# Performance work log

Hardware: AMD Instinct MI355X
Metric: run time of the kernel (lower is better)

Reference implementation:

```python
import jax, jax.numpy as jnp
import numpy as np

H = 128          # hidden_dim
L = 3            # num_layers
N = 100_000      # nodes
E = 1_600_000    # edges (avg degree 16)


def setup_inputs() -> dict:
    key = jax.random.key(0)
    ks = jax.random.split(key, 12)
    x = jax.random.normal(ks[0], (N, 5), dtype=jnp.float32)
    edge_index = jax.random.randint(ks[1], (2, E), 0, N, dtype=jnp.int64)
    edge_attr = jax.random.normal(ks[2], (E, 4), dtype=jnp.float32)

    def w(k, shape):
        fan_in = shape[-2]
        return (jax.random.normal(k, shape, dtype=jnp.float32) / np.sqrt(fan_in)).astype(jnp.float32)

    return {
        "x": x, "edge_index": edge_index, "edge_attr": edge_attr,
        # input_mlp: Linear(3,H) + SiLU
        "in_w": w(ks[3], (3, H)), "in_b": jnp.zeros((H,), jnp.float32),
        # per-layer edge_mlp: Linear(10,H) SiLU Linear(H,H), stacked over L layers
        "ew1": w(ks[4], (L, 10, H)), "eb1": jnp.zeros((L, H), jnp.float32),
        "ew2": w(ks[5], (L, H, H)), "eb2": jnp.zeros((L, H), jnp.float32),
        # per-layer node_mlp: Linear(2H,H) SiLU Linear(H,H)
        "nw1": w(ks[6], (L, 2 * H, H)), "nb1": jnp.zeros((L, H), jnp.float32),
        "nw2": w(ks[7], (L, H, H)), "nb2": jnp.zeros((L, H), jnp.float32),
        # output_mlp: Linear(H,H) SiLU Linear(H,1)
        "ow1": w(ks[8], (H, H)), "ob1": jnp.zeros((H,), jnp.float32),
        "ow2": w(ks[9], (H, 1)), "ob2": jnp.zeros((1,), jnp.float32),
    }


def reference(x, edge_index, edge_attr,
              in_w, in_b,
              ew1, eb1, ew2, eb2,
              nw1, nb1, nw2, nb2,
              ow1, ob1, ow2, ob2):
    n = x.shape[0]
    src, dst = edge_index[0], edge_index[1]  # PyG: j=src=edge_index[0], i=dst=edge_index[1]

    node_type = x[:, :2]
    spins = x[:, 2:5]
    # F.normalize(spins, dim=1) with eps=1e-12
    spins = spins / jnp.maximum(jnp.linalg.norm(spins, axis=-1, keepdims=True), 1e-12)
    spin_norm = jnp.linalg.norm(spins, axis=-1, keepdims=True)

    h = jax.nn.silu(jnp.concatenate([node_type, spin_norm], axis=-1) @ in_w + in_b)  # [N,H]

    # per-edge scalar invariants: layer-independent, compute once. [E,10]
    m_i, m_j = spins[dst], spins[src]
    nt_i, nt_j = node_type[dst], node_type[src]
    unit_vec = edge_attr[:, :3]
    distance = edge_attr[:, 3:4]
    scalars = jnp.concatenate([
        jnp.linalg.norm(m_i, axis=-1, keepdims=True),
        jnp.linalg.norm(m_j, axis=-1, keepdims=True),
        jnp.sum(m_i * m_j, axis=-1, keepdims=True),
        jnp.sum(m_i * unit_vec, axis=-1, keepdims=True),
        jnp.sum(m_j * unit_vec, axis=-1, keepdims=True),
        distance, nt_i, nt_j], axis=-1)

    def layer(h, p):
        w1, b1, w2, b2, mw1, mb1, mw2, mb2 = p
        msg = jax.nn.silu(scalars @ w1 + b1) @ w2 + b2            # [E,H] edge MLP
        aggr = jax.ops.segment_sum(msg, dst, num_segments=n)      # scatter-add to dst
        upd = jax.nn.silu(jnp.concatenate([h, aggr], -1) @ mw1 + mb1) @ mw2 + mb2
        return h + upd, None                                      # residual

    h, _ = jax.lax.scan(layer, h, (ew1, eb1, ew2, eb2, nw1, nb1, nw2, nb2))

    weights = jax.nn.silu(h @ ow1 + ob1) @ ow2 + ob2               # [N,1]
    contrib = weights[src] * spins[src]                            # [E,3]
    b_field = jax.ops.segment_sum(contrib, dst, num_segments=n)    # [N,3]
    return b_field
```

## Files before the change

kernel.cpp:

```cpp
#include <hip/hip_runtime.h>
#include <hip/hip_bf16.h>
#include <math.h>

typedef __attribute__((ext_vector_type(8))) short bf16x8;
typedef __attribute__((ext_vector_type(4))) float f32x4;
typedef __attribute__((ext_vector_type(4))) unsigned u32x4;

#define C_NLOG2E -1.4426950408889634f
#define C_NLN2   -0.6931471805599453f

__device__ __forceinline__ float silu_f(float x){
  return x * __builtin_amdgcn_rcpf(1.f + __expf(-x));
}

__device__ __forceinline__ void silu_acc(float h, float& s){
  float r = __builtin_amdgcn_rcpf(1.f + __builtin_amdgcn_exp2f(h));
  s = fmaf(h, r, s);
}

__device__ __forceinline__ short f2bs(float x){
  unsigned u = __builtin_bit_cast(unsigned, x);
  unsigned r = (u + 0x7fffu + ((u >> 16) & 1u)) >> 16;
  return (short)r;
}
__device__ __forceinline__ float bs2f(ushort u){
  unsigned v = ((unsigned)u) << 16;
  return __builtin_bit_cast(float, v);
}

__global__ void k_detect(const int* __restrict__ ei, int E, int* __restrict__ flag){
  __shared__ int nz;
  if (threadIdx.x==0) nz = 0;
  __syncthreads();
  int lim = E < 4096 ? E : 4096;
  int c = 0;
  for (int e = threadIdx.x; e < lim; e += blockDim.x)
    if (ei[2*e+1] != 0) c++;
  if (c) atomicAdd(&nz, c);
  __syncthreads();
  if (threadIdx.x==0) *flag = (nz==0) ? 1 : 0;
}

__global__ __launch_bounds__(256) void k_deg(const int* __restrict__ ei, int E,
                                             const int* __restrict__ flag, int* __restrict__ deg){
  int e = blockIdx.x*blockDim.x + threadIdx.x;
  if (e >= E) return;
  int d = (*flag) ? ei[2*(E+e)] : ei[E+e];
  atomicAdd(&deg[d], 1);
}

__global__ __launch_bounds__(256) void k_scan1(const int* __restrict__ deg, int* __restrict__ offs,
                                               int* __restrict__ bsum,
                                               const float* __restrict__ x, float4* __restrict__ nrec,
                                               int n){
  __shared__ int sh[256];
  int i = blockIdx.x*256 + threadIdx.x;
  int v = (i < n) ? deg[i] : 0;
  sh[threadIdx.x] = v;
  if (i < n){
    float nt0 = x[i*5+0], nt1 = x[i*5+1];
    float sx = x[i*5+2], sy = x[i*5+3], sz = x[i*5+4];
    float nrm = sqrtf(sx*sx + sy*sy + sz*sz);
    float d = fmaxf(nrm, 1e-12f);
    float mx = sx/d, my = sy/d, mz = sz/d;
    float rn = sqrtf(mx*mx + my*my + mz*mz);
    nrec[(size_t)i*2]   = make_float4(mx, my, mz, rn);
    nrec[(size_t)i*2+1] = make_float4(nt0, nt1, 0.f, 0.f);
  }
  __syncthreads();
  for (int off=1; off<256; off<<=1){
    int t = (threadIdx.x >= off) ? sh[threadIdx.x-off] : 0;
    __syncthreads();
    sh[threadIdx.x] += t;
    __syncthreads();
  }
  if (i < n) offs[i] = sh[threadIdx.x] - v;
  if (threadIdx.x == 255) bsum[blockIdx.x] = sh[255];
}

__global__ __launch_bounds__(512) void k_scan2(int* __restrict__ bsum, int nb){
  __shared__ int sh[512];
  int v = (threadIdx.x < nb) ? bsum[threadIdx.x] : 0;
  sh[threadIdx.x] = v;
  __syncthreads();
  for (int off=1; off<512; off<<=1){
    int t = (threadIdx.x >= off) ? sh[threadIdx.x-off] : 0;
    __syncthreads();
    sh[threadIdx.x] += t;
    __syncthreads();
  }
  if (threadIdx.x < nb) bsum[threadIdx.x] = sh[threadIdx.x] - v;
}

__global__ __launch_bounds__(256) void k_scan3(int* __restrict__ offs, const int* __restrict__ bsum,
                                               int* __restrict__ cursor,
                                               const int* __restrict__ deg,
                                               int* __restrict__ cnt, int4* __restrict__ c4,
                                               int4* __restrict__ c8, int n){
  int i = blockIdx.x*256 + threadIdx.x;
  if (i >= n) return;
  int o = offs[i] + bsum[i>>8];
  offs[i] = o;
  cursor[i] = o;
  int d = deg[i];
  int r = d & 15;
  if (r == 0 || r >= 9) return;
  int base = o + (d & ~15);
  if (r <= 4){
    int s = atomicAdd(&cnt[0], 1);
    c4[s] = make_int4(i, base, r, 0);
  } else {
    int s = atomicAdd(&cnt[1], 2);
    c8[s]   = make_int4(i, base, 4, 0);
    c8[s+1] = make_int4(i, base+4, r-4, 0);
  }
}

__global__ __launch_bounds__(256) void k_scatter(const int* __restrict__ ei, int E,
                                                 const int* __restrict__ flag,
                                                 const float* __restrict__ eattr,
                                                 const float4* __restrict__ nrec,
                                                 int* __restrict__ cursor,
                                                 int* __restrict__ srcS, ushort* __restrict__ scE){
  int e = blockIdx.x*blockDim.x + threadIdx.x;
  if (e >= E) return;
  int i64 = *flag;
  int s = i64 ? ei[2*e]       : ei[e];
  int d = i64 ? ei[2*(E+e)]   : ei[E+e];
  float4 ea = *(const float4*)(eattr + (size_t)e*4);
  float4 mi  = nrec[(size_t)d*2];
  float4 nti = nrec[(size_t)d*2+1];
  float4 mj  = nrec[(size_t)s*2];
  float4 ntj = nrec[(size_t)s*2+1];
  __align__(16) ushort row[16];
  row[0] = (ushort)f2bs(mi.w);
  row[1] = (ushort)f2bs(mj.w);
  row[2] = (ushort)f2bs(mi.x*mj.x + mi.y*mj.y + mi.z*mj.z);
  row[3] = (ushort)f2bs(mi.x*ea.x + mi.y*ea.y + mi.z*ea.z);
  row[4] = (ushort)f2bs(mj.x*ea.x + mj.y*ea.y + mj.z*ea.z);
  row[5] = (ushort)f2bs(ea.w);
  row[6] = (ushort)f2bs(nti.x);
  row[7] = (ushort)f2bs(nti.y);
  row[8] = (ushort)f2bs(ntj.x);
  row[9] = (ushort)f2bs(ntj.y);
  row[10]= 0x3F80;
  row[11]=0; row[12]=0; row[13]=0; row[14]=0; row[15]=0;
  int pos = atomicAdd(&cursor[d], 1);
  srcS[pos] = s;
  u32x4* dstp = (u32x4*)(scE + (size_t)pos*16);
  dstp[0] = *(u32x4*)row;
  dstp[1] = *(u32x4*)(row + 8);
}

__global__ __launch_bounds__(64) void k_pack(const float* __restrict__ ew2, const float* __restrict__ nw1,
                                             const float* __restrict__ nw2, const float* __restrict__ ow1,
                                             const float* __restrict__ ew1, const float* __restrict__ eb1,
                                             short* __restrict__ p_ew2, short* __restrict__ p_nw1,
                                             short* __restrict__ p_nw2, short* __restrict__ p_ow1,
                                             short* __restrict__ p_ew1){
  int b = blockIdx.x;
  int L = threadIdx.x;
  if (b >= 416){
    int tile = b - 416;
    int l = tile >> 3, t = tile & 7;
    int col = t*16 + (L & 15);
    int kb  = (L >> 4) << 3;
    __align__(16) short tmp[8];
    #pragma unroll
    for (int e=0;e<8;e++){
      int k = kb + e;
      float v = 0.f;
      if (k < 10)       v = ew1[(size_t)l*1280 + (size_t)k*128 + col];
      else if (k == 10) v = eb1[(size_t)l*128 + col];
      tmp[e] = f2bs(v * C_NLOG2E);
    }
    *(bf16x8*)(p_ew1 + (size_t)l*4096 + t*512 + L*8) = *(bf16x8*)tmp;
    return;
  }
  const float* src; short* dst; int tile;
  float sc = 1.f;
  if (b < 96){        int l = b>>5;              tile = b & 31; src = ew2 + (size_t)l*16384; dst = p_ew2 + (size_t)l*16384; sc = C_NLN2; }
  else if (b < 288){  int l = (b-96)>>6;         tile = (b-96) & 63; src = nw1 + (size_t)l*32768; dst = p_nw1 + (size_t)l*32768; }
  else if (b < 384){  int l = (b-288)>>5;        tile = (b-288) & 31; src = nw2 + (size_t)l*16384; dst = p_nw2 + (size_t)l*16384; }
  else {                                          tile = b - 384; src = ow1; dst = p_ow1; }
  int c = tile >> 3, t = tile & 7;
  int kb  = c*32 + ((L>>4)<<3);
  int col = t*16 + (L&15);
  __align__(16) short tmp[8];
  #pragma unroll
  for (int e=0;e<8;e++) tmp[e] = f2bs(src[(size_t)(kb+e)*128 + col] * sc);
  *(bf16x8*)(dst + ((size_t)tile*64 + L)*8) = *(bf16x8*)tmp;
}

__global__ __launch_bounds__(256) void k_edge3(
    const ushort* __restrict__ scE,
    const int* __restrict__ offs, const int* __restrict__ deg,
    const short* __restrict__ p_ew1,
    ushort* __restrict__ A, int n, size_t lstride){
  int wv = threadIdx.x >> 6, lane = threadIdx.x & 63;
  int i = blockIdx.x*4 + wv;
  if (i >= n) return;
  int quad = lane >> 4, lr = lane & 15;
  int p0 = __builtin_amdgcn_readfirstlane(offs[i]);
  int dg = __builtin_amdgcn_readfirstlane(deg[i]);
  int r  = dg & 15;
  int gfull = dg & ~15;
  const f32x4 zf = {0.f,0.f,0.f,0.f};
  const u32x4 z4 = {0u,0u,0u,0u};
  #pragma unroll 1
  for (int l=0; l<3; ++l){
    const short* pB = p_ew1 + (size_t)l*4096 + (size_t)lane*8;
    bf16x8 bfr[8];
    #pragma unroll
    for (int t=0;t<8;t++) bfr[t] = *(const bf16x8*)(pB + t*512);
    float s8[8];
    #pragma unroll
    for (int t=0;t<8;t++) s8[t] = 0.f;
    auto body = [&](u32x4 d4){
      bf16x8 af = __builtin_bit_cast(bf16x8, d4);
      #pragma unroll
      for (int t=0;t<8;t++){
        f32x4 acc = __builtin_amdgcn_mfma_f32_16x16x32_bf16(af, bfr[t], zf, 0, 0, 0);
        silu_acc(acc[0], s8[t]);
        silu_acc(acc[1], s8[t]);
        silu_acc(acc[2], s8[t]);
        silu_acc(acc[3], s8[t]);
      }
    };
    for (int g=0; g<gfull; g+=16){
      u32x4 d4 = z4;
      if (quad < 2)
        d4 = *(const u32x4*)(scE + ((size_t)(p0+g+lr))*16 + quad*8);
      body(d4);
    }
    if (r >= 9){
      int e = gfull + lr;
      u32x4 d4 = z4;
      if (quad < 2 && e < dg)
        d4 = *(const u32x4*)(scE + ((size_t)(p0+e))*16 + quad*8);
      body(d4);
    }
    #pragma unroll
    for (int t=0;t<8;t++){
      s8[t] += __shfl_xor(s8[t], 16, 64);
      s8[t] += __shfl_xor(s8[t], 32, 64);
    }
    if (quad == 0){
      #pragma unroll
      for (int t=0;t<8;t++)
        A[lstride*l + (size_t)i*128 + t*16 + lr] = (ushort)f2bs(s8[t]);
    }
  }
}

__global__ __launch_bounds__(256) void k_edge_rem(
    const ushort* __restrict__ scE,
    const int* __restrict__ cnt,
    const int4* __restrict__ c4, const int4* __restrict__ c8,
    const short* __restrict__ p_ew1,
    ushort* __restrict__ A, size_t lstride, int T4){
  int wave = threadIdx.x >> 6, lane = threadIdx.x & 63;
  int tw = blockIdx.x*4 + wave;
  const int4* slots;
  int mode;
  if (tw < T4){
    if (tw*4 >= cnt[0]) return;
    slots = c4 + (size_t)tw*4; mode = 0;
  } else {
    int t2 = tw - T4;
    if (t2*4 >= cnt[1]) return;
    slots = c8 + (size_t)t2*4; mode = 1;
  }
  int lr = lane & 15, quad = lane >> 4;
  int4 sl = slots[lr >> 2];
  int4 so = slots[quad];
  u32x4 d4 = {0u,0u,0u,0u};
  if (quad < 2 && (lr & 3) < sl.z)
    d4 = *(const u32x4*)(scE + (size_t)(sl.y + (lr & 3))*16 + quad*8);
  bf16x8 af = __builtin_bit_cast(bf16x8, d4);
  const f32x4 zf = {0.f,0.f,0.f,0.f};
  bool writer = (so.x >= 0) && (mode == 0 || (quad & 1) == 0);
  #pragma unroll 1
  for (int l=0; l<3; ++l){
    const short* pB = p_ew1 + (size_t)l*4096 + (size_t)lane*8;
    float s8[8];
    #pragma unroll
    for (int t=0;t<8;t++){
      bf16x8 bf = *(const bf16x8*)(pB + t*512);
      f32x4 acc = __builtin_amdgcn_mfma_f32_16x16x32_bf16(af, bf, zf, 0, 0, 0);
      float s = 0.f;
      silu_acc(acc[0], s);
      silu_acc(acc[1], s);
      silu_acc(acc[2], s);
      silu_acc(acc[3], s);
      s8[t] = s;
    }
    if (mode == 1){
      #pragma unroll
      for (int t=0;t<8;t++) s8[t] += __shfl_xor(s8[t], 16, 64);
    }
    if (writer){
      ushort* Ar = A + lstride*l + (size_t)so.x*128;
      #pragma unroll
      for (int t=0;t<8;t++){
        int col = t*16 + lr;
        Ar[col] = (ushort)f2bs(bs2f(Ar[col]) + s8[t]);
      }
    }
  }
}

__device__ __forceinline__ void wave_gemm2(const short* __restrict__ s0, const short* __restrict__ s1,
                                           const short* __restrict__ pw, int lane,
                                           f32x4 acc0[8], f32x4 acc1[8]){
  int lro = (lane & 15)*136 + ((lane >> 4) << 3);
  #pragma unroll
  for (int c=0;c<4;c++){
    bf16x8 a0 = *(const bf16x8*)(s0 + lro + c*32);
    bf16x8 a1 = *(const bf16x8*)(s1 + lro + c*32);
    const short* pB = pw + (size_t)c*4096 + (size_t)lane*8;
    #pragma unroll
    for (int t=0;t<8;t++){
      bf16x8 bf = *(const bf16x8*)(pB + t*512);
      acc0[t] = __builtin_amdgcn_mfma_f32_16x16x32_bf16(a0, bf, acc0[t], 0, 0, 0);
      acc1[t] = __builtin_amdgcn_mfma_f32_16x16x32_bf16(a1, bf, acc1[t], 0, 0, 0);
    }
  }
}

__global__ __launch_bounds__(64,2) void k_layers(
    const ushort* __restrict__ A, size_t lstride,
    const short* __restrict__ p_ew2, const float* __restrict__ eb2,
    const short* __restrict__ p_nw1, const float* __restrict__ nb1,
    const short* __restrict__ p_nw2, const float* __restrict__ nb2,
    const int* __restrict__ deg,
    const short* __restrict__ p_ow1, const float* __restrict__ ob1,
    const float* __restrict__ ow2, const float* __restrict__ ob2,
    const float* __restrict__ inw, const float* __restrict__ inb,
    const float4* __restrict__ nrec, float4* __restrict__ wspin, int n){
  __shared__ __align__(16) short sH[2][2176];
  __shared__ __align__(16) short sG[2][2176];
  int lane = threadIdx.x;
  int lr = lane & 15, quad = lane >> 4, qrow = quad << 2;
  int b0 = blockIdx.x*32;
  int b1 = b0 + 16;

  const f32x4 zf = {0.f,0.f,0.f,0.f};
  const bf16x8 zb = {0,0,0,0,0,0,0,0};
  f32x4 h0a[8], h1a[8];
  f32x4 acc0[8], acc1[8];
  bool rv0 = (b0 + lr) < n, rv1 = (b1 + lr) < n;
  float dd0[4], dd1[4];

  {
    float nt0a[4], nt1a[4], rna[4], nt0b[4], nt1b[4], rnb[4];
    #pragma unroll
    for (int r=0;r<4;r++){
      int ra = b0 + qrow + r, rb = b1 + qrow + r;
      if (ra < n){
        float4 a = nrec[(size_t)ra*2]; float4 b = nrec[(size_t)ra*2+1];
        nt0a[r]=b.x; nt1a[r]=b.y; rna[r]=a.w; dd0[r]=(float)deg[ra];
      } else { nt0a[r]=0.f; nt1a[r]=0.f; rna[r]=0.f; dd0[r]=0.f; }
      if (rb < n){
        float4 a = nrec[(size_t)rb*2]; float4 b = nrec[(size_t)rb*2+1];
        nt0b[r]=b.x; nt1b[r]=b.y; rnb[r]=a.w; dd1[r]=(float)deg[rb];
      } else { nt0b[r]=0.f; nt1b[r]=0.f; rnb[r]=0.f; dd1[r]=0.f; }
    }
    #pragma unroll
    for (int t=0;t<8;t++){
      int col = t*16 + lr;
      float w0=inw[col], w1=inw[128+col], w2=inw[256+col], bb=inb[col];
      #pragma unroll
      for (int r=0;r<4;r++){
        h0a[t][r] = silu_f(nt0a[r]*w0 + nt1a[r]*w1 + rna[r]*w2 + bb);
        h1a[t][r] = silu_f(nt0b[r]*w0 + nt1b[r]*w1 + rnb[r]*w2 + bb);
      }
    }
    #pragma unroll
    for (int t=0;t<8;t++){
      int col = t*16 + lr;
      #pragma unroll
      for (int r=0;r<4;r++){
        sH[0][(qrow+r)*136 + col] = f2bs(h0a[t][r]);
        sH[1][(qrow+r)*136 + col] = f2bs(h1a[t][r]);
      }
    }
  }

  #pragma unroll 1
  for (int l=0;l<3;++l){
    #pragma unroll
    for (int t=0;t<8;t++){ acc0[t] = zf; acc1[t] = zf; }
    {
      const ushort* gA0 = A + lstride*l + ((size_t)(b0 + lr))*128 + qrow*2;
      const ushort* gA1 = A + lstride*l + ((size_t)(b1 + lr))*128 + qrow*2;
      const short* pw = p_ew2 + (size_t)l*16384;
      #pragma unroll
      for (int c=0;c<4;c++){
        bf16x8 a0 = rv0 ? *(const bf16x8*)(gA0 + c*32) : zb;
        bf16x8 a1 = rv1 ? *(const bf16x8*)(gA1 + c*32) : zb;
        const short* pB = pw + (size_t)c*4096 + (size_t)lane*8;
        #pragma unroll
        for (int t=0;t<8;t++){
          bf16x8 bf = *(const bf16x8*)(pB + t*512);
          acc0[t] = __builtin_amdgcn_mfma_f32_16x16x32_bf16(a0, bf, acc0[t], 0, 0, 0);
          acc1[t] = __builtin_amdgcn_mfma_f32_16x16x32_bf16(a1, bf, acc1[t], 0, 0, 0);
        }
      }
    }
    {
      const float* eb2l = eb2 + l*128;
      #pragma unroll
      for (int t=0;t<8;t++){
        int col = t*16 + lr; float bv = eb2l[col];
        #pragma unroll
        for (int r=0;r<4;r++){
          sG[0][(qrow+r)*136 + col] = f2bs(acc0[t][r] + dd0[r]*bv);
          sG[1][(qrow+r)*136 + col] = f2bs(acc1[t][r] + dd1[r]*bv);
        }
      }
    }
    #pragma unroll
    for (int t=0;t<8;t++){ acc0[t] = zf; acc1[t] = zf; }
    wave_gemm2(sH[0], sH[1], p_nw1 + (size_t)l*32768,         lane, acc0, acc1);
    wave_gemm2(sG[0], sG[1], p_nw1 + (size_t)l*32768 + 16384, lane, acc0, acc1);
    {
      const float* nb1l = nb1 + l*128;
      #pragma unroll
      for (int t=0;t<8;t++){
        int col = t*16 + lr; float bv = nb1l[col];
        #pragma unroll
        for (int r=0;r<4;r++){
          sG[0][(qrow+r)*136 + col] = f2bs(silu_f(acc0[t][r] + bv));
          sG[1][(qrow+r)*136 + col] = f2bs(silu_f(acc1[t][r] + bv));
        }
      }
    }
    #pragma unroll
    for (int t=0;t<8;t++){ acc0[t] = zf; acc1[t] = zf; }
    wave_gemm2(sG[0], sG[1], p_nw2 + (size_t)l*16384, lane, acc0, acc1);
    {
      const float* nb2l = nb2 + l*128;
      #pragma unroll
      for (int t=0;t<8;t++){
        int col = t*16 + lr; float bv = nb2l[col];
        #pragma unroll
        for (int r=0;r<4;r++){
          h0a[t][r] += acc0[t][r] + bv;
          h1a[t][r] += acc1[t][r] + bv;
        }
      }
    }
    #pragma unroll
    for (int t=0;t<8;t++){
      int col = t*16 + lr;
      #pragma unroll
      for (int r=0;r<4;r++){
        sH[0][(qrow+r)*136 + col] = f2bs(h0a[t][r]);
        sH[1][(qrow+r)*136 + col] = f2bs(h1a[t][r]);
      }
    }
  }

  #pragma unroll
  for (int t=0;t<8;t++){ acc0[t] = zf; acc1[t] = zf; }
  wave_gemm2(sH[0], sH[1], p_ow1, lane, acc0, acc1);
  float p0[4] = {0.f,0.f,0.f,0.f}, p1[4] = {0.f,0.f,0.f,0.f};
  #pragma unroll
  for (int t=0;t<8;t++){
    int col = t*16 + lr;
    float bb = ob1[col], w2 = ow2[col];
    #pragma unroll
    for (int r=0;r<4;r++){
      p0[r] += silu_f(acc0[t][r] + bb)*w2;
      p1[r] += silu_f(acc1[t][r] + bb)*w2;
    }
  }
  #pragma unroll
  for (int m=1;m<16;m<<=1){
    #pragma unroll
    for (int r=0;r<4;r++){
      p0[r] += __shfl_xor(p0[r], m, 64);
      p1[r] += __shfl_xor(p1[r], m, 64);
    }
  }
  if (lr == 0){
    float b = ob2[0];
    #pragma unroll
    for (int r=0;r<4;r++){
      int ra = b0 + qrow + r;
      if (ra < n){
        float wv = p0[r] + b;
        float4 sp = nrec[(size_t)ra*2];
        wspin[ra] = make_float4(wv*sp.x, wv*sp.y, wv*sp.z, 0.f);
      }
      int rb = b1 + qrow + r;
      if (rb < n){
        float wv = p1[r] + b;
        float4 sp = nrec[(size_t)rb*2];
        wspin[rb] = make_float4(wv*sp.x, wv*sp.y, wv*sp.z, 0.f);
      }
    }
  }
}

__global__ __launch_bounds__(256) void k_bfield(const int* __restrict__ srcS,
                                                const float4* __restrict__ wspin,
                                                const int* __restrict__ offs,
                                                const int* __restrict__ deg, float* __restrict__ out, int n){
  int tid = threadIdx.x;
  int lr = tid & 15;
  int i = blockIdx.x*16 + (tid >> 4);
  if (i >= n) return;
  int p0 = offs[i], e = deg[i];
  float ax=0.f, ay=0.f, az=0.f;
  for (int q=lr; q<e; q+=16){
    int s = srcS[p0+q];
    float4 ws = wspin[s];
    ax += ws.x; ay += ws.y; az += ws.z;
  }
  #pragma unroll
  for (int m=1;m<16;m<<=1){
    ax += __shfl_xor(ax, m, 64);
    ay += __shfl_xor(ay, m, 64);
    az += __shfl_xor(az, m, 64);
  }
  if (lr == 0){
    out[(size_t)i*3+0] = ax;
    out[(size_t)i*3+1] = ay;
    out[(size_t)i*3+2] = az;
  }
}

extern "C" void kernel_launch(void* const* d_in, const int* in_sizes, int n_in,
                              void* d_out, int out_size, void* d_ws, size_t ws_size,
                              hipStream_t stream){
  const float* x      = (const float*)d_in[0];
  const int*   ei     = (const int*)  d_in[1];
  const float* eattr  = (const float*)d_in[2];
  const float* in_w   = (const float*)d_in[3];
  const float* in_b   = (const float*)d_in[4];
  const float* ew1    = (const float*)d_in[5];
  const float* eb1    = (const float*)d_in[6];
  const float* ew2    = (const float*)d_in[7];
  const float* eb2    = (const float*)d_in[8];
  const float* nw1    = (const float*)d_in[9];
  const float* nb1    = (const float*)d_in[10];
  const float* nw2    = (const float*)d_in[11];
  const float* nb2    = (const float*)d_in[12];
  const float* ow1    = (const float*)d_in[13];
  const float* ob1    = (const float*)d_in[14];
  const float* ow2    = (const float*)d_in[15];
  const float* ob2    = (const float*)d_in[16];
  float* out = (float*)d_out;

  const int N = in_sizes[0] / 5;
  const int E = in_sizes[1] / 2;
  const int T4 = (N + 3) / 4;
  const int T8 = (2*N + 3) / 4;

  char* w = (char*)d_ws;
  size_t off = 0;
  auto alloc = [&](size_t bytes)->size_t{
    size_t o = off; off = (off + bytes + 255) & ~(size_t)255; return o;
  };
  size_t o_flag   = alloc(4);
  size_t o_deg    = alloc((size_t)N*4);
  size_t o_offs   = alloc((size_t)N*4);
  size_t o_cursor = alloc((size_t)N*4);
  size_t o_bsum   = alloc(512*4);
  size_t o_nrec   = alloc((size_t)N*32);
  size_t o_wspin  = alloc((size_t)N*16);
  size_t o_A      = alloc((size_t)3*N*128*2);
  size_t o_pew2   = alloc((size_t)3*128*128*2);
  size_t o_pnw1   = alloc((size_t)3*256*128*2);
  size_t o_pnw2   = alloc((size_t)3*128*128*2);
  size_t o_pow1   = alloc((size_t)128*128*2);
  size_t o_pew1   = alloc((size_t)3*4096*2);
  size_t o_srcS   = alloc((size_t)E*4);
  size_t o_scE    = alloc((size_t)E*32);
  size_t o_cnt    = alloc(8);
  size_t o_c4     = alloc((size_t)T4*4*16);
  size_t o_c8     = alloc((size_t)T8*4*16);
  if (off > ws_size) return;

  int*    flag   = (int*)   (w + o_flag);
  int*    deg    = (int*)   (w + o_deg);
  int*    offs   = (int*)   (w + o_offs);
  int*    cursor = (int*)   (w + o_cursor);
  int*    bsum   = (int*)   (w + o_bsum);
  float4* nrec   = (float4*)(w + o_nrec);
  float4* wspin  = (float4*)(w + o_wspin);
  ushort* A      = (ushort*)(w + o_A);
  short*  p_ew2  = (short*) (w + o_pew2);
  short*  p_nw1  = (short*) (w + o_pnw1);
  short*  p_nw2  = (short*) (w + o_pnw2);
  short*  p_ow1  = (short*) (w + o_pow1);
  short*  p_ew1  = (short*) (w + o_pew1);
  int*    srcS   = (int*)   (w + o_srcS);
  ushort* scE    = (ushort*)(w + o_scE);
  int*    cnt    = (int*)   (w + o_cnt);
  int4*   c4s    = (int4*)  (w + o_c4);
  int4*   c8s    = (int4*)  (w + o_c8);

  (void)hipMemsetAsync(deg, 0, (size_t)N*4, stream);
  (void)hipMemsetAsync(cnt, 0, 8, stream);
  (void)hipMemsetAsync(c4s, 0xFF, (size_t)T4*4*16, stream);
  (void)hipMemsetAsync(c8s, 0xFF, (size_t)T8*4*16, stream);

  const int nb = (N + 255) / 256;
  const size_t lstride = (size_t)N*128;

  k_detect<<<1, 256, 0, stream>>>(ei, E, flag);
  k_deg<<<(E+255)/256, 256, 0, stream>>>(ei, E, flag, deg);
  k_scan1<<<nb, 256, 0, stream>>>(deg, offs, bsum, x, nrec, N);
  k_scan2<<<1, 512, 0, stream>>>(bsum, nb);
  k_scan3<<<nb, 256, 0, stream>>>(offs, bsum, cursor, deg, cnt, c4s, c8s, N);
  k_scatter<<<(E+255)/256, 256, 0, stream>>>(ei, E, flag, eattr, nrec, cursor, srcS, scE);
  k_pack<<<440, 64, 0, stream>>>(ew2, nw1, nw2, ow1, ew1, eb1,
                                 p_ew2, p_nw1, p_nw2, p_ow1, p_ew1);

  k_edge3<<<(N+3)/4, 256, 0, stream>>>(scE, offs, deg, p_ew1, A, N, lstride);
  k_edge_rem<<<(T4+T8+3)/4, 256, 0, stream>>>(scE, cnt, c4s, c8s, p_ew1, A, lstride, T4);

  k_layers<<<(N+31)/32, 64, 0, stream>>>(A, lstride, p_ew2, eb2, p_nw1, nb1, p_nw2, nb2,
                                         deg, p_ow1, ob1, ow2, ob2, in_w, in_b,
                                         nrec, wspin, N);

  k_bfield<<<(N+15)/16, 256, 0, stream>>>(srcS, wspin, offs, deg, out, N);
}
```

Baseline: 641.0 us.

## Permute hidden-column layout for packed bf16 vector stores and prefetch edge loads

Reorders the K dimension of the packed weight matrices so that each lane's eight MFMA output columns become contiguous in memory. That lets the intermediate activations (aggregates A, sH, sG) be written as one packed 16-byte store via v_cvt_pk_bf16_f32 instead of eight scattered 2-byte stores. It also software-pipelines the per-node edge loop so the next edge tile's load is issued before the current MFMA body runs. This touches weight packing, the producer kernels and the consumer reads together, so every component must agree on the permutation.

```diff
diff --git a/kernel.cpp b/kernel.cpp
--- a/kernel.cpp
+++ b/kernel.cpp
@@ -27,6 +27,14 @@
   unsigned v = ((unsigned)u) << 16;
   return __builtin_bit_cast(float, v);
 }
+
+__device__ __forceinline__ unsigned pk2(float a, float b){
+  unsigned r;
+  asm("v_cvt_pk_bf16_f32 %0, %1, %2" : "=v"(r) : "v"(a), "v"(b));
+  return r;
+}
+
+__device__ __forceinline__ int kperm(int k){ return ((k & 7) << 4) | (k >> 3); }
 
 __global__ void k_detect(const int* __restrict__ ei, int E, int* __restrict__ flag){
   __shared__ int nz;
@@ -188,7 +196,11 @@
   int col = t*16 + (L&15);
   __align__(16) short tmp[8];
   #pragma unroll
-  for (int e=0;e<8;e++) tmp[e] = f2bs(src[(size_t)(kb+e)*128 + col] * sc);
+  for (int e=0;e<8;e++){
+    int k = kb + e;
+    int kk = (k < 128) ? kperm(k) : 128 + kperm(k - 128);
+    tmp[e] = f2bs(src[(size_t)kk*128 + col] * sc);
+  }
   *(bf16x8*)(dst + ((size_t)tile*64 + L)*8) = *(bf16x8*)tmp;
 }
 
@@ -207,6 +219,7 @@
   int gfull = dg & ~15;
   const f32x4 zf = {0.f,0.f,0.f,0.f};
   const u32x4 z4 = {0u,0u,0u,0u};
+  const ushort* pE = scE + (size_t)(p0 + lr)*16 + quad*8;
   #pragma unroll 1
   for (int l=0; l<3; ++l){
     const short* pB = p_ew1 + (size_t)l*4096 + (size_t)lane*8;
@@ -227,28 +240,38 @@
         silu_acc(acc[3], s8[t]);
       }
     };
-    for (int g=0; g<gfull; g+=16){
-      u32x4 d4 = z4;
-      if (quad < 2)
-        d4 = *(const u32x4*)(scE + ((size_t)(p0+g+lr))*16 + quad*8);
-      body(d4);
-    }
-    if (r >= 9){
+    u32x4 tailv = z4;
+    if (r >= 9 && quad < 2){
       int e = gfull + lr;
-      u32x4 d4 = z4;
-      if (quad < 2 && e < dg)
-        d4 = *(const u32x4*)(scE + ((size_t)(p0+e))*16 + quad*8);
-      body(d4);
-    }
+      if (e < dg) tailv = *(const u32x4*)(pE + (size_t)gfull*16);
+    }
+    u32x4 cur = tailv;
+    if (gfull > 0){
+      cur = z4;
+      if (quad < 2) cur = *(const u32x4*)(pE);
+    }
+    for (int g = 16; g <= gfull; g += 16){
+      u32x4 nxt = tailv;
+      if (g < gfull){
+        nxt = z4;
+        if (quad < 2) nxt = *(const u32x4*)(pE + (size_t)g*16);
+      }
+      body(cur);
+      cur = nxt;
+    }
+    if (r >= 9) body(cur);
     #pragma unroll
     for (int t=0;t<8;t++){
       s8[t] += __shfl_xor(s8[t], 16, 64);
       s8[t] += __shfl_xor(s8[t], 32, 64);
     }
     if (quad == 0){
-      #pragma unroll
-      for (int t=0;t<8;t++)
-        A[lstride*l + (size_t)i*128 + t*16 + lr] = (ushort)f2bs(s8[t]);
+      u32x4 q;
+      q[0] = pk2(s8[0], s8[1]);
+      q[1] = pk2(s8[2], s8[3]);
+      q[2] = pk2(s8[4], s8[5]);
+      q[3] = pk2(s8[6], s8[7]);
+      *(u32x4*)(A + lstride*l + (size_t)i*128 + lr*8) = q;
     }
   }
 }
@@ -303,8 +326,8 @@
       ushort* Ar = A + lstride*l + (size_t)so.x*128;
       #pragma unroll
       for (int t=0;t<8;t++){
-        int col = t*16 + lr;
-        Ar[col] = (ushort)f2bs(bs2f(Ar[col]) + s8[t]);
+        int p = lr*8 + t;
+        Ar[p] = (ushort)f2bs(bs2f(Ar[p]) + s8[t]);
       }
     }
   }
@@ -352,6 +375,15 @@
   bool rv0 = (b0 + lr) < n, rv1 = (b1 + lr) < n;
   float dd0[4], dd1[4];
 
+  auto st_row = [&](short* base, int row, const float v[8]){
+    u32x4 q;
+    q[0] = pk2(v[0], v[1]);
+    q[1] = pk2(v[2], v[3]);
+    q[2] = pk2(v[4], v[5]);
+    q[3] = pk2(v[6], v[7]);
+    *(u32x4*)(base + row*136 + lr*8) = q;
+  };
+
   {
     float nt0a[4], nt1a[4], rna[4], nt0b[4], nt1b[4], rnb[4];
     #pragma unroll
@@ -377,13 +409,12 @@
       }
     }
     #pragma unroll
-    for (int t=0;t<8;t++){
-      int col = t*16 + lr;
-      #pragma unroll
-      for (int r=0;r<4;r++){
-        sH[0][(qrow+r)*136 + col] = f2bs(h0a[t][r]);
-        sH[1][(qrow+r)*136 + col] = f2bs(h1a[t][r]);
-      }
+    for (int r=0;r<4;r++){
+      float va[8], vb[8];
+      #pragma unroll
+      for (int t=0;t<8;t++){ va[t] = h0a[t][r]; vb[t] = h1a[t][r]; }
+      st_row(sH[0], qrow+r, va);
+      st_row(sH[1], qrow+r, vb);
     }
   }
 
@@ -410,14 +441,19 @@
     }
     {
       const float* eb2l = eb2 + l*128;
-      #pragma unroll
-      for (int t=0;t<8;t++){
-        int col = t*16 + lr; float bv = eb2l[col];
+      float bv[8];
+      #pragma unroll
+      for (int t=0;t<8;t++) bv[t] = eb2l[t*16 + lr];
+      #pragma unroll
+      for (int r=0;r<4;r++){
+        float va[8], vb[8];
         #pragma unroll
-        for (int r=0;r<4;r++){
-          sG[0][(qrow+r)*136 + col] = f2bs(acc0[t][r] + dd0[r]*bv);
-          sG[1][(qrow+r)*136 + col] = f2bs(acc1[t][r] + dd1[r]*bv);
+        for (int t=0;t<8;t++){
+          va[t] = acc0[t][r] + dd0[r]*bv[t];
+          vb[t] = acc1[t][r] + dd1[r]*bv[t];
         }
+        st_row(sG[0], qrow+r, va);
+        st_row(sG[1], qrow+r, vb);
       }
     }
     #pragma unroll
@@ -426,14 +462,19 @@
     wave_gemm2(sG[0], sG[1], p_nw1 + (size_t)l*32768 + 16384, lane, acc0, acc1);
     {
       const float* nb1l = nb1 + l*128;
-      #pragma unroll
-      for (int t=0;t<8;t++){
-        int col = t*16 + lr; float bv = nb1l[col];
+      float bv[8];
+      #pragma unroll
+      for (int t=0;t<8;t++) bv[t] = nb1l[t*16 + lr];
+      #pragma unroll
+      for (int r=0;r<4;r++){
+        float va[8], vb[8];
         #pragma unroll
-        for (int r=0;r<4;r++){
-          sG[0][(qrow+r)*136 + col] = f2bs(silu_f(acc0[t][r] + bv));
-          sG[1][(qrow+r)*136 + col] = f2bs(silu_f(acc1[t][r] + bv));
+        for (int t=0;t<8;t++){
+          va[t] = silu_f(acc0[t][r] + bv[t]);
+          vb[t] = silu_f(acc1[t][r] + bv[t]);
         }
+        st_row(sG[0], qrow+r, va);
+        st_row(sG[1], qrow+r, vb);
       }
     }
     #pragma unroll
@@ -452,13 +493,12 @@
       }
     }
     #pragma unroll
-    for (int t=0;t<8;t++){
-      int col = t*16 + lr;
-      #pragma unroll
-      for (int r=0;r<4;r++){
-        sH[0][(qrow+r)*136 + col] = f2bs(h0a[t][r]);
-        sH[1][(qrow+r)*136 + col] = f2bs(h1a[t][r]);
-      }
+    for (int r=0;r<4;r++){
+      float va[8], vb[8];
+      #pragma unroll
+      for (int t=0;t<8;t++){ va[t] = h0a[t][r]; vb[t] = h1a[t][r]; }
+      st_row(sH[0], qrow+r, va);
+      st_row(sH[1], qrow+r, vb);
     }
   }
 
```

Result: slower. 737.4 us (+15.0%).
